# Kernel optimization log

Hardware: AMD Instinct MI355X
Metric: run time of the kernel (lower is better)

The kernel has to match this reference:

```python
import jax, jax.numpy as jnp
import numpy as np

CHAMFER_WEIGHT = 1.0
PC_NUM_WEIGHT = 0.1


def setup_inputs() -> dict:
    key = jax.random.key(0)
    k1, k2, k3, k4, k5 = jax.random.split(key, 5)
    B, D, H, W = 4, 20, 128, 128
    pred_coor = jax.random.normal(k1, (B, 3 * D, H, W), dtype=jnp.float32)
    gt_coor = jax.random.normal(k2, (B, D, 3, H, W), dtype=jnp.float32)
    chamfer_mask = (jax.random.uniform(k3, (B, D, H, W)) < 0.7).astype(jnp.float32)
    gt_mask = jnp.ones((B, H, W), dtype=jnp.float32)
    pred_num = jax.random.normal(k4, (B, 1, H, W), dtype=jnp.float32)
    gt_num = jax.random.normal(k5, (B, 1, H, W), dtype=jnp.float32)
    return {"pred_coor": pred_coor, "gt_coor": gt_coor, "chamfer_mask": chamfer_mask,
            "gt_mask": gt_mask, "pred_num": pred_num, "gt_num": gt_num}


def _chamfer(pred_coor, gt_coor, chamfer_mask, gt_mask):
    B, _, H, W = pred_coor.shape
    D = gt_coor.shape[1]
    # src: [B,3*D,H,W] -> [K,3,D] -> [K,D,3]  (matches torch reshape(-1,3,20).permute(0,2,1))
    src = pred_coor.transpose(0, 2, 3, 1).reshape(-1, 3, D).transpose(0, 2, 1)
    # dst: [B,D,3,H,W] -> [B,D*3,H,W] -> [K,D,3]
    dst = gt_coor.reshape(B, D * 3, H, W).transpose(0, 2, 3, 1).reshape(-1, D, 3)
    cm = chamfer_mask.transpose(0, 2, 3, 1).reshape(-1, D)  # [K,D]
    vw = gt_mask.reshape(-1)  # [K] voxel selection weight (binary)

    # L1 pairwise distance, summed over coordinate axis: [K,D,D]
    dist = jnp.abs(src[:, :, None, :] - dst[:, None, :, :]).sum(-1)
    max_d = jax.lax.stop_gradient(
        jnp.max(jnp.where(vw[:, None, None] > 0, dist, -jnp.inf)))
    s2d = jnp.min(dist - cm[:, None, :] * max_d, axis=2) + max_d  # [K,D]
    d2s = jnp.min(dist, axis=1)                                    # [K,D]

    wsum = vw.sum()
    loss_src = (s2d * vw[:, None]).sum() / (wsum * D)             # mean over selected
    denom = (cm * vw[:, None]).sum()
    loss_dst = (d2s * cm * vw[:, None]).sum() / denom
    return loss_src + loss_dst


def _num_loss(pred_num, gt_num, gt_mask):
    diff = pred_num - gt_num
    ad = jnp.abs(diff)
    sl1 = jnp.where(ad < 1.0, 0.5 * diff * diff, ad - 0.5)  # smooth_l1, beta=1
    sl1 = sl1.squeeze(1)  # [B,H,W]
    return (sl1 * gt_mask).sum() / gt_mask.sum()


def reference(pred_coor, gt_coor, chamfer_mask, gt_mask, pred_num, gt_num):
    chamfer_loss = _chamfer(pred_coor, gt_coor, chamfer_mask, gt_mask)
    pc_num_loss = _num_loss(pred_num, gt_num, gt_mask)
    return CHAMFER_WEIGHT * chamfer_loss + PC_NUM_WEIGHT * pc_num_loss
```

## Files before the change

kernel.cpp:

```cpp
#include <hip/hip_runtime.h>
#include <stdint.h>

#define HW   16384
#define VPB  64
#define NBLK 1024

#define OFF_PRED 0
#define OFF_GT   3840
#define OFF_CM   7680
#define OFF_RMM  0
#define OFF_RMA  2560
#define OFF_D2S  5120
#define OFF_MX   8960
#define SMEM_F   9216

__device__ __forceinline__ void gload_lds16(const float* g, float* l) {
    __builtin_amdgcn_global_load_lds(
        (const __attribute__((address_space(1))) uint32_t*)g,
        (__attribute__((address_space(3))) uint32_t*)l, 16, 0, 0);
}

__global__ __launch_bounds__(256, 4) void chamfer_main(
    const float* __restrict__ pred,
    const float* __restrict__ gt,
    const float* __restrict__ cmask,
    const float* __restrict__ vmask,
    const float* __restrict__ pnum,
    const float* __restrict__ gnum,
    float* __restrict__ ws)
{
    __shared__ float smem[SMEM_F];
    const int lane = threadIdx.x & 63;
    const int w    = threadIdx.x >> 6;
    const int ri   = w >> 1;
    const int cj   = w & 1;
    const int k    = blockIdx.x * VPB + lane;
    const int b    = k >> 14;
    const int hw0  = (blockIdx.x * VPB) & (HW - 1);
    const float* gb = pred  + (size_t)b * 60 * HW + hw0;
    const float* tb = gt    + (size_t)b * 60 * HW + hw0;
    const float* cb = cmask + (size_t)b * 20 * HW + hw0;

    {
        const int sub = lane >> 4;
        const int vo  = (lane & 15) * 4;
        for (int t = w; t < 35; t += 4) {
            const float* src; int ch0, region;
            if (t < 15)      { src = gb; ch0 = t * 4;        region = OFF_PRED; }
            else if (t < 30) { src = tb; ch0 = (t - 15) * 4; region = OFF_GT;   }
            else             { src = cb; ch0 = (t - 30) * 4; region = OFF_CM;   }
            gload_lds16(src + (size_t)(ch0 + sub) * HW + vo,
                        &smem[region + ch0 * 64]);
        }
    }
    float vw = 0.f, pn = 0.f, gn = 0.f;
    if (w == 0) { vw = vmask[k]; pn = pnum[k]; gn = gnum[k]; }
    asm volatile("s_waitcnt vmcnt(0)" ::: "memory");
    __syncthreads();

    const int j0 = cj * 10, i0 = ri * 10;
    float dx[10], dy[10], dz[10];
    #pragma unroll
    for (int jj = 0; jj < 10; ++jj) {
        dx[jj] = smem[OFF_GT + (3 * (j0 + jj)    ) * 64 + lane];
        dy[jj] = smem[OFF_GT + (3 * (j0 + jj) + 1) * 64 + lane];
        dz[jj] = smem[OFF_GT + (3 * (j0 + jj) + 2) * 64 + lane];
    }
    unsigned mybits = 0u;
    #pragma unroll
    for (int jj = 0; jj < 10; ++jj)
        if (smem[OFF_CM + (j0 + jj) * 64 + lane] > 0.f) mybits |= 1u << jj;

    const float INF = __int_as_float(0x7f800000);
    float d2s[10], rmm[10], rma[10], locmax = 0.f;
    #pragma unroll
    for (int t = 0; t < 10; ++t) { d2s[t] = INF; rmm[t] = INF; rma[t] = INF; }

    #pragma unroll
    for (int r = 0; r < 10; ++r) {
        const int i = i0 + r;
        const float sx = smem[OFF_PRED + (i)      * 64 + lane];
        const float sy = smem[OFF_PRED + (20 + i) * 64 + lane];
        const float sz = smem[OFF_PRED + (40 + i) * 64 + lane];
        #pragma unroll
        for (int jj = 0; jj < 10; ++jj) {
            float d = fabsf(sx - dx[jj]) + fabsf(sy - dy[jj]) + fabsf(sz - dz[jj]);
            locmax  = fmaxf(locmax, d);
            d2s[jj] = fminf(d2s[jj], d);
            rma[r]  = fminf(rma[r], d);
            rmm[r]  = fminf(rmm[r], ((mybits >> jj) & 1u) ? d : INF);
        }
    }
    __syncthreads();

    #pragma unroll
    for (int r = 0; r < 10; ++r) {
        smem[OFF_RMM + ((i0 + r) * 2 + cj) * 64 + lane] = rmm[r];
        smem[OFF_RMA + ((i0 + r) * 2 + cj) * 64 + lane] = rma[r];
        smem[OFF_D2S + ((j0 + r) * 2 + ri) * 64 + lane] = d2s[r];
    }
    smem[OFF_MX + w * 64 + lane] = locmax;
    __syncthreads();

    if (w == 0) {
        unsigned cmbits = 0u;
        #pragma unroll
        for (int j = 0; j < 20; ++j)
            if (smem[OFF_CM + j * 64 + lane] > 0.f) cmbits |= 1u << j;
        const int selbase = cmbits ? OFF_RMM : OFF_RMA;
        float srcA = 0.f;
        #pragma unroll
        for (int i = 0; i < 20; ++i)
            srcA += fminf(smem[selbase + (i * 2)     * 64 + lane],
                          smem[selbase + (i * 2 + 1) * 64 + lane]);
        float dsum = 0.f;
        #pragma unroll
        for (int j = 0; j < 20; ++j) {
            float m = fminf(smem[OFF_D2S + (j * 2)     * 64 + lane],
                            smem[OFF_D2S + (j * 2 + 1) * 64 + lane]);
            if ((cmbits >> j) & 1u) dsum += m;
        }
        float mx = fmaxf(fmaxf(smem[OFF_MX + lane],       smem[OFF_MX + 64 + lane]),
                         fmaxf(smem[OFF_MX + 128 + lane], smem[OFF_MX + 192 + lane]));

        float vals[7];
        vals[0] = srcA * vw;
        vals[1] = (cmbits == 0u) ? 20.f * vw : 0.f;
        vals[2] = dsum * vw;
        vals[3] = vw * (float)__popc(cmbits);
        const float diff = pn - gn;
        const float ad = fabsf(diff);
        vals[4] = ((ad < 1.f) ? 0.5f * diff * diff : (ad - 0.5f)) * vw;
        vals[5] = vw;
        vals[6] = (vw > 0.f) ? mx : 0.f;

        #pragma unroll
        for (int o = 32; o > 0; o >>= 1) {
            #pragma unroll
            for (int x = 0; x < 6; ++x) vals[x] += __shfl_down(vals[x], o);
            vals[6] = fmaxf(vals[6], __shfl_down(vals[6], o));
        }
        if (lane == 0) {
            float* rec = ws + (size_t)blockIdx.x * 8;
            #pragma unroll
            for (int x = 0; x < 7; ++x) rec[x] = vals[x];
        }
    }
}

__global__ __launch_bounds__(64) void chamfer_fin(
    const float* __restrict__ ws, float* __restrict__ out)
{
    const int t = threadIdx.x;
    float a[6] = {0.f, 0.f, 0.f, 0.f, 0.f, 0.f};
    float mx = 0.f;
    for (int r = t; r < NBLK; r += 64) {
        const float* rec = ws + (size_t)r * 8;
        #pragma unroll
        for (int v = 0; v < 6; ++v) a[v] += rec[v];
        mx = fmaxf(mx, rec[6]);
    }
    #pragma unroll
    for (int o = 32; o > 0; o >>= 1) {
        #pragma unroll
        for (int v = 0; v < 6; ++v) a[v] += __shfl_down(a[v], o);
        mx = fmaxf(mx, __shfl_down(mx, o));
    }
    if (t == 0) {
        const float loss_s = (a[0] + a[1] * mx) / (a[5] * 20.f);
        const float loss_d = a[2] / a[3];
        const float numl   = a[4] / a[5];
        out[0] = loss_s + loss_d + 0.1f * numl;
    }
}

extern "C" void kernel_launch(void* const* d_in, const int* in_sizes, int n_in,
                              void* d_out, int out_size, void* d_ws, size_t ws_size,
                              hipStream_t stream)
{
    const float* pred  = (const float*)d_in[0];
    const float* gt    = (const float*)d_in[1];
    const float* cmask = (const float*)d_in[2];
    const float* vmask = (const float*)d_in[3];
    const float* pnum  = (const float*)d_in[4];
    const float* gnum  = (const float*)d_in[5];
    float* out = (float*)d_out;
    float* ws  = (float*)d_ws;

    const int nvox = in_sizes[3];
    chamfer_main<<<nvox / VPB, 256, 0, stream>>>(pred, gt, cmask, vmask, pnum, gnum, ws);
    chamfer_fin<<<1, 64, 0, stream>>>(ws, out);
}
```

Before: 22.06 us.

## Process two voxel tiles per block with double-buffered LDS staging

Each block now handles two 64-voxel tiles and issues both tiles' global-to-LDS loads up front. It computes the first tile while the second is still in flight, using partial vmcnt waits. The gt coordinates are loaded straight into registers instead of going through LDS, and the separate rma array is dropped by picking the row-min selection mask ahead of time. The cost is half as many blocks (512), a hardcoded tile count, a larger LDS footprint, and higher register pressure under a 2-wave occupancy bound.

```diff
diff --git a/kernel.cpp b/kernel.cpp
--- a/kernel.cpp
+++ b/kernel.cpp
@@ -1,18 +1,23 @@
 #include <hip/hip_runtime.h>
 #include <stdint.h>
 
-#define HW   16384
-#define VPB  64
-#define NBLK 1024
-
-#define OFF_PRED 0
-#define OFF_GT   3840
-#define OFF_CM   7680
-#define OFF_RMM  0
-#define OFF_RMA  2560
-#define OFF_D2S  5120
-#define OFF_MX   8960
-#define SMEM_F   9216
+#define HW      16384
+#define NBLOCKS 512
+#define NTILES  1024
+
+#define STG0   0
+#define STG1   5120
+#define RMMo   10240
+#define D2So   12800
+#define MXo    15360
+#define SMEM_F 15616
+
+#define MEMBAR()  asm volatile("" ::: "memory")
+#define WAITV35() asm volatile("s_waitcnt vmcnt(35)" ::: "memory")
+#define WAITV0()  asm volatile("s_waitcnt vmcnt(0)" ::: "memory")
+#define WAITL0()  asm volatile("s_waitcnt lgkmcnt(0)" ::: "memory")
+#define SBAR() do { __builtin_amdgcn_sched_barrier(0); __builtin_amdgcn_s_barrier(); \
+                    __builtin_amdgcn_sched_barrier(0); } while (0)
 
 __device__ __forceinline__ void gload_lds16(const float* g, float* l) {
     __builtin_amdgcn_global_load_lds(
@@ -20,7 +25,103 @@
         (__attribute__((address_space(3))) uint32_t*)l, 16, 0, 0);
 }
 
-__global__ __launch_bounds__(256, 4) void chamfer_main(
+__device__ __forceinline__ void stage_tile(float* smem, int stg, int lane, int w,
+                                           const float* pb, const float* cb)
+{
+    const int sub = lane >> 4;
+    const int vo  = (lane & 15) * 4;
+    #pragma unroll
+    for (int q = 0; q < 5; ++q) {
+        const int t   = w + q * 4;
+        const int ch0 = t * 4;
+        const float* src = (ch0 < 60) ? (pb + (size_t)(ch0 + sub) * HW + vo)
+                                      : (cb + (size_t)(ch0 - 60 + sub) * HW + vo);
+        gload_lds16(src, &smem[stg + ch0 * 64]);
+    }
+}
+
+__device__ __forceinline__ void compute_tile(float* smem, int stg, int lane,
+    int w, int ri, int cj,
+    const float (&dx)[10], const float (&dy)[10], const float (&dz)[10],
+    unsigned& cmbits_out)
+{
+    const int j0 = cj * 10, i0 = ri * 10;
+    unsigned cmbits = 0u;
+    #pragma unroll
+    for (int j = 0; j < 20; ++j)
+        if (smem[stg + (60 + j) * 64 + lane] > 0.f) cmbits |= 1u << j;
+    const unsigned sel = cmbits ? ((cmbits >> j0) & 0x3FFu) : 0x3FFu;
+
+    const float INF = __int_as_float(0x7f800000);
+    float rmm[10], d2s[10], mx = 0.f;
+    #pragma unroll
+    for (int t = 0; t < 10; ++t) { rmm[t] = INF; d2s[t] = INF; }
+
+    #pragma unroll
+    for (int r = 0; r < 10; ++r) {
+        const int i = i0 + r;
+        const float sx = smem[stg + (i)      * 64 + lane];
+        const float sy = smem[stg + (20 + i) * 64 + lane];
+        const float sz = smem[stg + (40 + i) * 64 + lane];
+        #pragma unroll
+        for (int jj = 0; jj < 10; ++jj) {
+            float d = fabsf(sx - dx[jj]) + fabsf(sy - dy[jj]) + fabsf(sz - dz[jj]);
+            mx      = fmaxf(mx, d);
+            d2s[jj] = fminf(d2s[jj], d);
+            rmm[r]  = fminf(rmm[r], ((sel >> jj) & 1u) ? d : INF);
+        }
+    }
+    #pragma unroll
+    for (int t = 0; t < 10; ++t) {
+        smem[RMMo + ((i0 + t) * 2 + cj) * 64 + lane] = rmm[t];
+        smem[D2So + ((j0 + t) * 2 + ri) * 64 + lane] = d2s[t];
+    }
+    smem[MXo + w * 64 + lane] = mx;
+    cmbits_out = cmbits;
+}
+
+__device__ __forceinline__ void finalize_tile(const float* smem, int lane,
+    unsigned cmbits, float vw, float pn, float gn, float* rec)
+{
+    float srcA = 0.f;
+    #pragma unroll
+    for (int i = 0; i < 20; ++i)
+        srcA += fminf(smem[RMMo + (i * 2)     * 64 + lane],
+                      smem[RMMo + (i * 2 + 1) * 64 + lane]);
+    float dsum = 0.f;
+    #pragma unroll
+    for (int j = 0; j < 20; ++j) {
+        float m = fminf(smem[D2So + (j * 2)     * 64 + lane],
+                        smem[D2So + (j * 2 + 1) * 64 + lane]);
+        if ((cmbits >> j) & 1u) dsum += m;
+    }
+    float mx = fmaxf(fmaxf(smem[MXo + lane],       smem[MXo + 64 + lane]),
+                     fmaxf(smem[MXo + 128 + lane], smem[MXo + 192 + lane]));
+
+    float vals[7];
+    vals[0] = srcA * vw;
+    vals[1] = (cmbits == 0u) ? 20.f * vw : 0.f;
+    vals[2] = dsum * vw;
+    vals[3] = vw * (float)__popc(cmbits);
+    const float diff = pn - gn;
+    const float ad = fabsf(diff);
+    vals[4] = ((ad < 1.f) ? 0.5f * diff * diff : (ad - 0.5f)) * vw;
+    vals[5] = vw;
+    vals[6] = (vw > 0.f) ? mx : 0.f;
+
+    #pragma unroll
+    for (int o = 32; o > 0; o >>= 1) {
+        #pragma unroll
+        for (int x = 0; x < 6; ++x) vals[x] += __shfl_down(vals[x], o);
+        vals[6] = fmaxf(vals[6], __shfl_down(vals[6], o));
+    }
+    if (lane == 0) {
+        #pragma unroll
+        for (int x = 0; x < 7; ++x) rec[x] = vals[x];
+    }
+}
+
+__global__ __launch_bounds__(256, 2) void chamfer_main(
     const float* __restrict__ pred,
     const float* __restrict__ gt,
     const float* __restrict__ cmask,
@@ -30,122 +131,63 @@
     float* __restrict__ ws)
 {
     __shared__ float smem[SMEM_F];
-    const int lane = threadIdx.x & 63;
-    const int w    = threadIdx.x >> 6;
+    const int tid  = threadIdx.x;
+    const int lane = tid & 63;
+    const int w    = tid >> 6;
     const int ri   = w >> 1;
     const int cj   = w & 1;
-    const int k    = blockIdx.x * VPB + lane;
-    const int b    = k >> 14;
-    const int hw0  = (blockIdx.x * VPB) & (HW - 1);
-    const float* gb = pred  + (size_t)b * 60 * HW + hw0;
-    const float* tb = gt    + (size_t)b * 60 * HW + hw0;
-    const float* cb = cmask + (size_t)b * 20 * HW + hw0;
-
-    {
-        const int sub = lane >> 4;
-        const int vo  = (lane & 15) * 4;
-        for (int t = w; t < 35; t += 4) {
-            const float* src; int ch0, region;
-            if (t < 15)      { src = gb; ch0 = t * 4;        region = OFF_PRED; }
-            else if (t < 30) { src = tb; ch0 = (t - 15) * 4; region = OFF_GT;   }
-            else             { src = cb; ch0 = (t - 30) * 4; region = OFF_CM;   }
-            gload_lds16(src + (size_t)(ch0 + sub) * HW + vo,
-                        &smem[region + ch0 * 64]);
-        }
-    }
-    float vw = 0.f, pn = 0.f, gn = 0.f;
-    if (w == 0) { vw = vmask[k]; pn = pnum[k]; gn = gnum[k]; }
-    asm volatile("s_waitcnt vmcnt(0)" ::: "memory");
-    __syncthreads();
-
-    const int j0 = cj * 10, i0 = ri * 10;
-    float dx[10], dy[10], dz[10];
+    const int j0   = cj * 10;
+
+    const int tA = blockIdx.x, tB = blockIdx.x + NBLOCKS;
+    const int kA = tA * 64, kB = tB * 64;
+    const int bA = kA >> 14, hwA = kA & (HW - 1);
+    const int bB = kB >> 14, hwB = kB & (HW - 1);
+    const float* pbA = pred  + (size_t)bA * 60 * HW + hwA;
+    const float* tbA = gt    + (size_t)bA * 60 * HW + hwA;
+    const float* cbA = cmask + (size_t)bA * 20 * HW + hwA;
+    const float* pbB = pred  + (size_t)bB * 60 * HW + hwB;
+    const float* tbB = gt    + (size_t)bB * 60 * HW + hwB;
+    const float* cbB = cmask + (size_t)bB * 20 * HW + hwB;
+
+    const float vwA = vmask[kA + lane], pnA = pnum[kA + lane], gnA = gnum[kA + lane];
+    const float vwB = vmask[kB + lane], pnB = pnum[kB + lane], gnB = gnum[kB + lane];
+    float dxa[10], dya[10], dza[10];
     #pragma unroll
     for (int jj = 0; jj < 10; ++jj) {
-        dx[jj] = smem[OFF_GT + (3 * (j0 + jj)    ) * 64 + lane];
-        dy[jj] = smem[OFF_GT + (3 * (j0 + jj) + 1) * 64 + lane];
-        dz[jj] = smem[OFF_GT + (3 * (j0 + jj) + 2) * 64 + lane];
-    }
-    unsigned mybits = 0u;
-    #pragma unroll
-    for (int jj = 0; jj < 10; ++jj)
-        if (smem[OFF_CM + (j0 + jj) * 64 + lane] > 0.f) mybits |= 1u << jj;
-
-    const float INF = __int_as_float(0x7f800000);
-    float d2s[10], rmm[10], rma[10], locmax = 0.f;
-    #pragma unroll
-    for (int t = 0; t < 10; ++t) { d2s[t] = INF; rmm[t] = INF; rma[t] = INF; }
-
-    #pragma unroll
-    for (int r = 0; r < 10; ++r) {
-        const int i = i0 + r;
-        const float sx = smem[OFF_PRED + (i)      * 64 + lane];
-        const float sy = smem[OFF_PRED + (20 + i) * 64 + lane];
-        const float sz = smem[OFF_PRED + (40 + i) * 64 + lane];
-        #pragma unroll
-        for (int jj = 0; jj < 10; ++jj) {
-            float d = fabsf(sx - dx[jj]) + fabsf(sy - dy[jj]) + fabsf(sz - dz[jj]);
-            locmax  = fmaxf(locmax, d);
-            d2s[jj] = fminf(d2s[jj], d);
-            rma[r]  = fminf(rma[r], d);
-            rmm[r]  = fminf(rmm[r], ((mybits >> jj) & 1u) ? d : INF);
-        }
-    }
-    __syncthreads();
-
-    #pragma unroll
-    for (int r = 0; r < 10; ++r) {
-        smem[OFF_RMM + ((i0 + r) * 2 + cj) * 64 + lane] = rmm[r];
-        smem[OFF_RMA + ((i0 + r) * 2 + cj) * 64 + lane] = rma[r];
-        smem[OFF_D2S + ((j0 + r) * 2 + ri) * 64 + lane] = d2s[r];
-    }
-    smem[OFF_MX + w * 64 + lane] = locmax;
-    __syncthreads();
-
-    if (w == 0) {
-        unsigned cmbits = 0u;
-        #pragma unroll
-        for (int j = 0; j < 20; ++j)
-            if (smem[OFF_CM + j * 64 + lane] > 0.f) cmbits |= 1u << j;
-        const int selbase = cmbits ? OFF_RMM : OFF_RMA;
-        float srcA = 0.f;
-        #pragma unroll
-        for (int i = 0; i < 20; ++i)
-            srcA += fminf(smem[selbase + (i * 2)     * 64 + lane],
-                          smem[selbase + (i * 2 + 1) * 64 + lane]);
-        float dsum = 0.f;
-        #pragma unroll
-        for (int j = 0; j < 20; ++j) {
-            float m = fminf(smem[OFF_D2S + (j * 2)     * 64 + lane],
-                            smem[OFF_D2S + (j * 2 + 1) * 64 + lane]);
-            if ((cmbits >> j) & 1u) dsum += m;
-        }
-        float mx = fmaxf(fmaxf(smem[OFF_MX + lane],       smem[OFF_MX + 64 + lane]),
-                         fmaxf(smem[OFF_MX + 128 + lane], smem[OFF_MX + 192 + lane]));
-
-        float vals[7];
-        vals[0] = srcA * vw;
-        vals[1] = (cmbits == 0u) ? 20.f * vw : 0.f;
-        vals[2] = dsum * vw;
-        vals[3] = vw * (float)__popc(cmbits);
-        const float diff = pn - gn;
-        const float ad = fabsf(diff);
-        vals[4] = ((ad < 1.f) ? 0.5f * diff * diff : (ad - 0.5f)) * vw;
-        vals[5] = vw;
-        vals[6] = (vw > 0.f) ? mx : 0.f;
-
-        #pragma unroll
-        for (int o = 32; o > 0; o >>= 1) {
-            #pragma unroll
-            for (int x = 0; x < 6; ++x) vals[x] += __shfl_down(vals[x], o);
-            vals[6] = fmaxf(vals[6], __shfl_down(vals[6], o));
-        }
-        if (lane == 0) {
-            float* rec = ws + (size_t)blockIdx.x * 8;
-            #pragma unroll
-            for (int x = 0; x < 7; ++x) rec[x] = vals[x];
-        }
-    }
+        dxa[jj] = tbA[(size_t)(3 * (j0 + jj)    ) * HW + lane];
+        dya[jj] = tbA[(size_t)(3 * (j0 + jj) + 1) * HW + lane];
+        dza[jj] = tbA[(size_t)(3 * (j0 + jj) + 2) * HW + lane];
+    }
+    MEMBAR();
+    stage_tile(smem, STG0, lane, w, pbA, cbA);
+    MEMBAR();
+    float dxb[10], dyb[10], dzb[10];
+    #pragma unroll
+    for (int jj = 0; jj < 10; ++jj) {
+        dxb[jj] = tbB[(size_t)(3 * (j0 + jj)    ) * HW + lane];
+        dyb[jj] = tbB[(size_t)(3 * (j0 + jj) + 1) * HW + lane];
+        dzb[jj] = tbB[(size_t)(3 * (j0 + jj) + 2) * HW + lane];
+    }
+    MEMBAR();
+    stage_tile(smem, STG1, lane, w, pbB, cbB);
+
+    WAITV35();
+    SBAR();
+
+    unsigned cmA;
+    compute_tile(smem, STG0, lane, w, ri, cj, dxa, dya, dza, cmA);
+    WAITL0();
+    SBAR();
+    if (w == 0) finalize_tile(smem, lane, cmA, vwA, pnA, gnA, ws + (size_t)tA * 8);
+
+    WAITV0();
+    SBAR();
+
+    unsigned cmB;
+    compute_tile(smem, STG1, lane, w, ri, cj, dxb, dyb, dzb, cmB);
+    WAITL0();
+    SBAR();
+    if (w == 0) finalize_tile(smem, lane, cmB, vwB, pnB, gnB, ws + (size_t)tB * 8);
 }
 
 __global__ __launch_bounds__(64) void chamfer_fin(
@@ -154,7 +196,7 @@
     const int t = threadIdx.x;
     float a[6] = {0.f, 0.f, 0.f, 0.f, 0.f, 0.f};
     float mx = 0.f;
-    for (int r = t; r < NBLK; r += 64) {
+    for (int r = t; r < NTILES; r += 64) {
         const float* rec = ws + (size_t)r * 8;
         #pragma unroll
         for (int v = 0; v < 6; ++v) a[v] += rec[v];
@@ -187,7 +229,6 @@
     float* out = (float*)d_out;
     float* ws  = (float*)d_ws;
 
-    const int nvox = in_sizes[3];
-    chamfer_main<<<nvox / VPB, 256, 0, stream>>>(pred, gt, cmask, vmask, pnum, gnum, ws);
+    chamfer_main<<<NBLOCKS, 256, 0, stream>>>(pred, gt, cmask, vmask, pnum, gnum, ws);
     chamfer_fin<<<1, 64, 0, stream>>>(ws, out);
 }
```

Result: slower. 23.70 us (+7.4%).

## Split voxel pairs across eight waves with direct loads and LDS atomic reductions

Applied to the files above, without the earlier changes.

The main kernel now runs 512 threads per block, splitting the 20x20 pair grid into 2x4 wave tiles (10 src rows by 5 dst columns) instead of 2x2. Each wave loads its gt, mask and pred values straight from global memory into registers, replacing the global-to-LDS staging. Partial row/column minima and the max are merged with integer LDS atomicMin/atomicMax on float bit patterns, and the mask bits are combined with atomicOr. This aims for more parallelism and lower register pressure per thread, at the cost of LDS atomics, an extra init pass, and redundant global loads of pred across the column waves. The final reduction kernel also moves to 256 threads.

```diff
diff --git a/kernel.cpp b/kernel.cpp
--- a/kernel.cpp
+++ b/kernel.cpp
@@ -1,26 +1,11 @@
 #include <hip/hip_runtime.h>
 #include <stdint.h>
 
-#define HW   16384
-#define VPB  64
-#define NBLK 1024
+#define HW     16384
+#define NTILES 1024
+#define INFI   0x7f800000
 
-#define OFF_PRED 0
-#define OFF_GT   3840
-#define OFF_CM   7680
-#define OFF_RMM  0
-#define OFF_RMA  2560
-#define OFF_D2S  5120
-#define OFF_MX   8960
-#define SMEM_F   9216
-
-__device__ __forceinline__ void gload_lds16(const float* g, float* l) {
-    __builtin_amdgcn_global_load_lds(
-        (const __attribute__((address_space(1))) uint32_t*)g,
-        (__attribute__((address_space(3))) uint32_t*)l, 16, 0, 0);
-}
-
-__global__ __launch_bounds__(256, 4) void chamfer_main(
+__global__ __launch_bounds__(512, 6) void chamfer_main(
     const float* __restrict__ pred,
     const float* __restrict__ gt,
     const float* __restrict__ cmask,
@@ -29,99 +14,96 @@
     const float* __restrict__ gnum,
     float* __restrict__ ws)
 {
-    __shared__ float smem[SMEM_F];
-    const int lane = threadIdx.x & 63;
-    const int w    = threadIdx.x >> 6;
-    const int ri   = w >> 1;
-    const int cj   = w & 1;
-    const int k    = blockIdx.x * VPB + lane;
+    __shared__ int rm_m[20][64];
+    __shared__ int rm_a[20][64];
+    __shared__ int cd_s[20][64];
+    __shared__ int mx_s[64];
+    __shared__ int bt_s[64];
+
+    const int tid  = threadIdx.x;
+    const int lane = tid & 63;
+    const int w    = tid >> 6;
+    const int ri   = w >> 2;
+    const int cj   = w & 3;
+    const int i0   = ri * 10, j0 = cj * 5;
+    const int k    = blockIdx.x * 64 + lane;
     const int b    = k >> 14;
-    const int hw0  = (blockIdx.x * VPB) & (HW - 1);
-    const float* gb = pred  + (size_t)b * 60 * HW + hw0;
-    const float* tb = gt    + (size_t)b * 60 * HW + hw0;
-    const float* cb = cmask + (size_t)b * 20 * HW + hw0;
+    const int hw   = k & (HW - 1);
+    const size_t pb = (size_t)b * 60 * HW + hw;
+    const size_t cb = (size_t)b * 20 * HW + hw;
 
-    {
-        const int sub = lane >> 4;
-        const int vo  = (lane & 15) * 4;
-        for (int t = w; t < 35; t += 4) {
-            const float* src; int ch0, region;
-            if (t < 15)      { src = gb; ch0 = t * 4;        region = OFF_PRED; }
-            else if (t < 30) { src = tb; ch0 = (t - 15) * 4; region = OFF_GT;   }
-            else             { src = cb; ch0 = (t - 30) * 4; region = OFF_CM;   }
-            gload_lds16(src + (size_t)(ch0 + sub) * HW + vo,
-                        &smem[region + ch0 * 64]);
-        }
+    float dxv[5], dyv[5], dzv[5], cmf[5];
+    #pragma unroll
+    for (int jj = 0; jj < 5; ++jj) {
+        dxv[jj] = gt[pb + (size_t)(3 * (j0 + jj)    ) * HW];
+        dyv[jj] = gt[pb + (size_t)(3 * (j0 + jj) + 1) * HW];
+        dzv[jj] = gt[pb + (size_t)(3 * (j0 + jj) + 2) * HW];
+        cmf[jj] = cmask[cb + (size_t)(j0 + jj) * HW];
     }
     float vw = 0.f, pn = 0.f, gn = 0.f;
     if (w == 0) { vw = vmask[k]; pn = pnum[k]; gn = gnum[k]; }
-    asm volatile("s_waitcnt vmcnt(0)" ::: "memory");
+
+    {
+        int* pm = &rm_m[0][0]; int* pa = &rm_a[0][0]; int* pc = &cd_s[0][0];
+        for (int t = tid; t < 1280; t += 512) { pm[t] = INFI; pa[t] = INFI; pc[t] = INFI; }
+        if (tid < 64) { mx_s[tid] = 0; bt_s[tid] = 0; }
+    }
     __syncthreads();
 
-    const int j0 = cj * 10, i0 = ri * 10;
-    float dx[10], dy[10], dz[10];
-    #pragma unroll
-    for (int jj = 0; jj < 10; ++jj) {
-        dx[jj] = smem[OFF_GT + (3 * (j0 + jj)    ) * 64 + lane];
-        dy[jj] = smem[OFF_GT + (3 * (j0 + jj) + 1) * 64 + lane];
-        dz[jj] = smem[OFF_GT + (3 * (j0 + jj) + 2) * 64 + lane];
-    }
     unsigned mybits = 0u;
     #pragma unroll
-    for (int jj = 0; jj < 10; ++jj)
-        if (smem[OFF_CM + (j0 + jj) * 64 + lane] > 0.f) mybits |= 1u << jj;
+    for (int jj = 0; jj < 5; ++jj)
+        if (cmf[jj] > 0.f) mybits |= 1u << jj;
+    if (ri == 0 && mybits) atomicOr(&bt_s[lane], (int)(mybits << j0));
 
-    const float INF = __int_as_float(0x7f800000);
-    float d2s[10], rmm[10], rma[10], locmax = 0.f;
+    const float INF = __int_as_float(INFI);
+    float rmm[10], rma[10], cds[5], mx = 0.f;
     #pragma unroll
-    for (int t = 0; t < 10; ++t) { d2s[t] = INF; rmm[t] = INF; rma[t] = INF; }
+    for (int t = 0; t < 10; ++t) { rmm[t] = INF; rma[t] = INF; }
+    #pragma unroll
+    for (int t = 0; t < 5; ++t) cds[t] = INF;
 
     #pragma unroll
     for (int r = 0; r < 10; ++r) {
         const int i = i0 + r;
-        const float sx = smem[OFF_PRED + (i)      * 64 + lane];
-        const float sy = smem[OFF_PRED + (20 + i) * 64 + lane];
-        const float sz = smem[OFF_PRED + (40 + i) * 64 + lane];
+        const float sx = pred[pb + (size_t)(i)      * HW];
+        const float sy = pred[pb + (size_t)(20 + i) * HW];
+        const float sz = pred[pb + (size_t)(40 + i) * HW];
         #pragma unroll
-        for (int jj = 0; jj < 10; ++jj) {
-            float d = fabsf(sx - dx[jj]) + fabsf(sy - dy[jj]) + fabsf(sz - dz[jj]);
-            locmax  = fmaxf(locmax, d);
-            d2s[jj] = fminf(d2s[jj], d);
+        for (int jj = 0; jj < 5; ++jj) {
+            float d = fabsf(sx - dxv[jj]) + fabsf(sy - dyv[jj]) + fabsf(sz - dzv[jj]);
+            mx      = fmaxf(mx, d);
+            cds[jj] = fminf(cds[jj], d);
             rma[r]  = fminf(rma[r], d);
-            rmm[r]  = fminf(rmm[r], ((mybits >> jj) & 1u) ? d : INF);
+            rmm[r]  = fminf(rmm[r], (cmf[jj] > 0.f) ? d : INF);
         }
     }
-    __syncthreads();
 
     #pragma unroll
     for (int r = 0; r < 10; ++r) {
-        smem[OFF_RMM + ((i0 + r) * 2 + cj) * 64 + lane] = rmm[r];
-        smem[OFF_RMA + ((i0 + r) * 2 + cj) * 64 + lane] = rma[r];
-        smem[OFF_D2S + ((j0 + r) * 2 + ri) * 64 + lane] = d2s[r];
+        atomicMin(&rm_m[i0 + r][lane], __float_as_int(rmm[r]));
+        atomicMin(&rm_a[i0 + r][lane], __float_as_int(rma[r]));
     }
-    smem[OFF_MX + w * 64 + lane] = locmax;
+    #pragma unroll
+    for (int jj = 0; jj < 5; ++jj)
+        atomicMin(&cd_s[j0 + jj][lane], __float_as_int(cds[jj]));
+    atomicMax(&mx_s[lane], __float_as_int(mx));
     __syncthreads();
 
     if (w == 0) {
-        unsigned cmbits = 0u;
+        const unsigned cmbits = (unsigned)bt_s[lane];
+        float srcA = 0.f;
+        #pragma unroll
+        for (int i = 0; i < 20; ++i) {
+            const int vm_ = rm_m[i][lane];
+            const int va_ = rm_a[i][lane];
+            srcA += __int_as_float(cmbits ? vm_ : va_);
+        }
+        float dsum = 0.f;
         #pragma unroll
         for (int j = 0; j < 20; ++j)
-            if (smem[OFF_CM + j * 64 + lane] > 0.f) cmbits |= 1u << j;
-        const int selbase = cmbits ? OFF_RMM : OFF_RMA;
-        float srcA = 0.f;
-        #pragma unroll
-        for (int i = 0; i < 20; ++i)
-            srcA += fminf(smem[selbase + (i * 2)     * 64 + lane],
-                          smem[selbase + (i * 2 + 1) * 64 + lane]);
-        float dsum = 0.f;
-        #pragma unroll
-        for (int j = 0; j < 20; ++j) {
-            float m = fminf(smem[OFF_D2S + (j * 2)     * 64 + lane],
-                            smem[OFF_D2S + (j * 2 + 1) * 64 + lane]);
-            if ((cmbits >> j) & 1u) dsum += m;
-        }
-        float mx = fmaxf(fmaxf(smem[OFF_MX + lane],       smem[OFF_MX + 64 + lane]),
-                         fmaxf(smem[OFF_MX + 128 + lane], smem[OFF_MX + 192 + lane]));
+            if ((cmbits >> j) & 1u) dsum += __int_as_float(cd_s[j][lane]);
+        const float mxv = __int_as_float(mx_s[lane]);
 
         float vals[7];
         vals[0] = srcA * vw;
@@ -132,7 +114,7 @@
         const float ad = fabsf(diff);
         vals[4] = ((ad < 1.f) ? 0.5f * diff * diff : (ad - 0.5f)) * vw;
         vals[5] = vw;
-        vals[6] = (vw > 0.f) ? mx : 0.f;
+        vals[6] = (vw > 0.f) ? mxv : 0.f;
 
         #pragma unroll
         for (int o = 32; o > 0; o >>= 1) {
@@ -148,13 +130,16 @@
     }
 }
 
-__global__ __launch_bounds__(64) void chamfer_fin(
+__global__ __launch_bounds__(256) void chamfer_fin(
     const float* __restrict__ ws, float* __restrict__ out)
 {
-    const int t = threadIdx.x;
+    __shared__ float red[4][8];
+    const int tid  = threadIdx.x;
+    const int lane = tid & 63;
+    const int wv   = tid >> 6;
     float a[6] = {0.f, 0.f, 0.f, 0.f, 0.f, 0.f};
     float mx = 0.f;
-    for (int r = t; r < NBLK; r += 64) {
+    for (int r = tid; r < NTILES; r += 256) {
         const float* rec = ws + (size_t)r * 8;
         #pragma unroll
         for (int v = 0; v < 6; ++v) a[v] += rec[v];
@@ -166,7 +151,16 @@
         for (int v = 0; v < 6; ++v) a[v] += __shfl_down(a[v], o);
         mx = fmaxf(mx, __shfl_down(mx, o));
     }
-    if (t == 0) {
+    if (lane == 0) {
+        #pragma unroll
+        for (int v = 0; v < 6; ++v) red[wv][v] = a[v];
+        red[wv][6] = mx;
+    }
+    __syncthreads();
+    if (tid == 0) {
+        #pragma unroll
+        for (int v = 0; v < 6; ++v) a[v] = red[0][v] + red[1][v] + red[2][v] + red[3][v];
+        mx = fmaxf(fmaxf(red[0][6], red[1][6]), fmaxf(red[2][6], red[3][6]));
         const float loss_s = (a[0] + a[1] * mx) / (a[5] * 20.f);
         const float loss_d = a[2] / a[3];
         const float numl   = a[4] / a[5];
@@ -187,7 +181,6 @@
     float* out = (float*)d_out;
     float* ws  = (float*)d_ws;
 
-    const int nvox = in_sizes[3];
-    chamfer_main<<<nvox / VPB, 256, 0, stream>>>(pred, gt, cmask, vmask, pnum, gnum, ws);
-    chamfer_fin<<<1, 64, 0, stream>>>(ws, out);
+    chamfer_main<<<NTILES, 512, 0, stream>>>(pred, gt, cmask, vmask, pnum, gnum, ws);
+    chamfer_fin<<<1, 256, 0, stream>>>(ws, out);
 }
```

After: 18.28 us. 1.21x faster.
